# Kernel tuning notes

Hardware: AMD Instinct MI355X
Metric: run time of the kernel (lower is better)

Reference implementation:

```python
import jax, jax.numpy as jnp
import numpy as np

HEADS = 3
NEG_SLOPE = 0.2


def setup_inputs() -> dict:
    key = jax.random.key(0)
    ks = jax.random.split(key, 16)
    B, node_num, his, in_dim = 2, 5000, 12, 2
    N = B * node_num
    E = 160000
    hidden = 32
    C = hidden * his  # 384, per-head out channels of GATConv
    gat_in = in_dim * his  # 24
    s = 0.05
    return {
        "x": jax.random.normal(ks[0], (B, node_num, his, in_dim), jnp.float32),
        "edge_index": jax.random.randint(ks[1], (2, E), 0, N, jnp.int64),
        "lin_w": jax.random.normal(ks[2], (HEADS * C, gat_in), jnp.float32) * s,
        "att_src": jax.random.normal(ks[3], (HEADS, C), jnp.float32) * s,
        "att_dst": jax.random.normal(ks[4], (HEADS, C), jnp.float32) * s,
        "gat_bias": jax.random.normal(ks[5], (C,), jnp.float32) * s,
        "w_ih": jax.random.normal(ks[6], (3 * hidden, hidden), jnp.float32) * s,
        "w_hh": jax.random.normal(ks[7], (3 * hidden, hidden), jnp.float32) * s,
        "b_ih": jax.random.normal(ks[8], (3 * hidden,), jnp.float32) * s,
        "b_hh": jax.random.normal(ks[9], (3 * hidden,), jnp.float32) * s,
        "p1_w": jax.random.normal(ks[10], (1, hidden), jnp.float32) * s,
        "p1_b": jax.random.normal(ks[11], (1,), jnp.float32) * s,
        "p2_w": jax.random.normal(ks[12], (his, his), jnp.float32) * s,
        "p2_b": jax.random.normal(ks[13], (his,), jnp.float32) * s,
    }


def _gat_conv(xf, src, dst, N, lin_w, att_src, att_dst, gat_bias):
    # xf: [N, gat_in]; returns [N, C] (mean over heads, concat=False)
    heads, C = att_src.shape
    h = (xf @ lin_w.T).reshape(N, heads, C)           # [N,heads,C]
    a_src = jnp.einsum('nhc,hc->nh', h, att_src)      # [N,heads]
    a_dst = jnp.einsum('nhc,hc->nh', h, att_dst)
    alpha = jax.nn.leaky_relu(a_src[src] + a_dst[dst], NEG_SLOPE)  # [E,heads]
    # edge softmax over incoming edges of each dst node (stable)
    amax = jax.ops.segment_max(alpha, dst, num_segments=N)
    ea = jnp.exp(alpha - amax[dst])
    denom = jax.ops.segment_sum(ea, dst, num_segments=N)
    w = ea / denom[dst]                               # [E,heads]
    msg = h[src] * w[:, :, None]                      # [E,heads,C] -- dominant traffic
    out = jax.ops.segment_sum(msg, dst, num_segments=N)
    return out.mean(axis=1) + gat_bias                # [N,C]


def _gru(seq, w_ih, w_hh, b_ih, b_hh):
    # seq: [N, T, H] -> outputs [N, T, H], PyTorch GRU gate order (r,z,n)
    N, T, H = seq.shape
    def step(hprev, xt):
        gi = xt @ w_ih.T + b_ih
        gh = hprev @ w_hh.T + b_hh
        ir, iz, inn = jnp.split(gi, 3, axis=-1)
        hr, hz, hn = jnp.split(gh, 3, axis=-1)
        r = jax.nn.sigmoid(ir + hr)
        z = jax.nn.sigmoid(iz + hz)
        n = jnp.tanh(inn + r * hn)
        hnew = (1.0 - z) * n + z * hprev
        return hnew, hnew
    h0 = jnp.zeros((N, H), seq.dtype)
    _, hs = jax.lax.scan(step, h0, seq.transpose(1, 0, 2))
    return hs.transpose(1, 0, 2)


def reference(x, edge_index, lin_w, att_src, att_dst, gat_bias,
              w_ih, w_hh, b_ih, b_hh, p1_w, p1_b, p2_w, p2_b):
    B, node_num, his, in_dim = x.shape
    N = B * node_num
    xf = x.reshape(N, his * in_dim)
    # GATConv adds self-loops (add_self_loops=True default in PyG)
    loops = jnp.arange(N)
    src = jnp.concatenate([edge_index[0], loops])
    dst = jnp.concatenate([edge_index[1], loops])
    gat_out = _gat_conv(xf, src, dst, N, lin_w, att_src, att_dst, gat_bias)  # [N, hidden*his]
    hidden = w_hh.shape[1]
    gru_in = gat_out.reshape(N, his, hidden)
    gru_out = _gru(gru_in, w_ih, w_hh, b_ih, b_hh)    # [N, his, hidden]
    o = (gru_out @ p1_w.T + p1_b).squeeze(-1)         # [N, his]
    o = o @ p2_w.T + p2_b                              # [N, pred_num]
    return o.reshape(B, node_num, -1)
```

## Files before the change

### kernel.cpp

```cpp
#include <hip/hip_runtime.h>
#include <math.h>

#define HEADS 3
#define C_OUT 384
#define GAT_IN 24
#define HID 32
#define TSTEPS 12
#define NEG_SLOPE 0.2f
#define CAPW 64
#define SLOTS 96

typedef __attribute__((ext_vector_type(8))) short bf16x8;
typedef __attribute__((ext_vector_type(4))) float f32x4;

__device__ __forceinline__ float sigm(float x) {
  return 1.f / (1.f + __expf(-x));
}
__device__ __forceinline__ float tanh_fast(float x) {
  return 2.f / (1.f + __expf(-2.f * x)) - 1.f;
}
__device__ __forceinline__ unsigned short f2bf(float x) {
  unsigned int u = __float_as_uint(x);
  unsigned int r = u + 0x7fffu + ((u >> 16) & 1u);
  return (unsigned short)(r >> 16);
}
__device__ __forceinline__ unsigned int packbf(float lo, float hi) {
  return (unsigned int)f2bf(lo) | ((unsigned int)f2bf(hi) << 16);
}
__device__ __forceinline__ float bf_lo(unsigned int u) {
  return __uint_as_float(u << 16);
}
__device__ __forceinline__ float bf_hi(unsigned int u) {
  return __uint_as_float(u & 0xffff0000u);
}
__device__ __forceinline__ float bf2f(unsigned short u) {
  return __uint_as_float((unsigned int)u << 16);
}
__device__ __forceinline__ float lrelu(float x) {
  return x >= 0.f ? x : NEG_SLOPE * x;
}

__global__ __launch_bounds__(96) void k_const(const float* __restrict__ lin_w,
                                              const float* __restrict__ gat_bias,
                                              const float* __restrict__ wih,
                                              const float* __restrict__ bih,
                                              const float* __restrict__ att_src,
                                              const float* __restrict__ att_dst,
                                              unsigned short* __restrict__ WWf,
                                              float* __restrict__ biasb,
                                              float* __restrict__ vbuf,
                                              int* __restrict__ cnt, int N) {
  int b = blockIdx.x;
  if (b < 876) {
    int t = b / 73, kk = b % 73;
    int g = threadIdx.x;
    __shared__ float s_w[32];
    if (g < 32) {
      if (kk < 72) {
        int h = kk / 24, j = kk % 24;
        s_w[g] = lin_w[(size_t)(h * C_OUT + t * 32 + g) * GAT_IN + j] * (1.f / 3.f);
      } else {
        s_w[g] = gat_bias[t * 32 + g];
      }
    }
    __syncthreads();
    const float* wrow = wih + (size_t)g * 32;
    float acc = 0.f;
#pragma unroll
    for (int c = 0; c < 32; ++c) acc += s_w[c] * wrow[c];
    int nt = g >> 4, c2 = g & 15;
    if (kk < 72) {
      int q = kk >> 5, rem = kk & 31, hi2 = rem >> 3, j2 = rem & 7;
      WWf[((((size_t)t * 3 + q) * 6 + nt) * 64 + hi2 * 16 + c2) * 8 + j2] =
          f2bf(acc);
      if (kk < 24) {
        int remz = kk + 8, hiz = remz >> 3, jz = remz & 7;
        WWf[((((size_t)t * 3 + 2) * 6 + nt) * 64 + hiz * 16 + c2) * 8 + jz] = 0;
      }
    } else {
      biasb[t * 96 + g] = acc + bih[g];
    }
  } else if (b < 948) {
    int bb = b - 876;
    int h = bb / 24, j = bb % 24;
    int lane = threadIdx.x;
    if (lane >= 64) return;
    float as = 0.f, ad = 0.f;
    for (int c = lane; c < C_OUT; c += 64) {
      float wv = lin_w[(size_t)(h * C_OUT + c) * GAT_IN + j];
      as += att_src[h * C_OUT + c] * wv;
      ad += att_dst[h * C_OUT + c] * wv;
    }
#pragma unroll
    for (int off = 32; off >= 1; off >>= 1) {
      as += __shfl_xor(as, off, 64);
      ad += __shfl_xor(ad, off, 64);
    }
    if (lane == 0) {
      vbuf[h * 24 + j] = as;
      vbuf[72 + h * 24 + j] = ad;
    }
  } else {
    int i = (b - 948) * 96 + threadIdx.x;
    if (i < N) cnt[i] = 0;
  }
}

__global__ void k_place(const int* __restrict__ esrc,
                        const int* __restrict__ edst, int* __restrict__ cnt,
                        int* __restrict__ slist, int E, int ET) {
  int e = blockIdx.x * blockDim.x + threadIdx.x;
  if (e >= ET) return;
  int d, s;
  if (e < E) { d = edst[e]; s = esrc[e]; }
  else { d = e - E; s = e - E; }
  int pos = atomicAdd(&cnt[d], 1);
  if (pos < SLOTS) slist[(size_t)d * SLOTS + pos] = s;
}

__global__ __launch_bounds__(256) void k_aggx(
    const float* __restrict__ xf, const float* __restrict__ vbuf,
    const int* __restrict__ slist, const int* __restrict__ cnt,
    unsigned short* __restrict__ Yb, int N) {
  __shared__ float s_v[144];
  __shared__ float s_w[4][CAPW][3];
  __shared__ unsigned short s_xb[4][CAPW][26];
  int tid = threadIdx.x, lane = tid & 63, wv = tid >> 6;
  if (tid < 144) s_v[tid] = vbuf[tid];
  __syncthreads();
  int n = blockIdx.x * 4 + wv;
  if (n >= N) return;

  int deg = min(cnt[n], SLOTS);

  float xl = (lane < 24) ? xf[(size_t)n * 24 + lane] : 0.f;
  float ad0, ad1, ad2;
  {
    float p0 = (lane < 24) ? xl * s_v[72 + lane] : 0.f;
    float p1 = (lane < 24) ? xl * s_v[96 + lane] : 0.f;
    float p2 = (lane < 24) ? xl * s_v[120 + lane] : 0.f;
#pragma unroll
    for (int off = 32; off >= 1; off >>= 1) {
      p0 += __shfl_xor(p0, off, 64);
      p1 += __shfl_xor(p1, off, 64);
      p2 += __shfl_xor(p2, off, 64);
    }
    ad0 = p0; ad1 = p1; ad2 = p2;
  }

  float t0 = 0.f, t1 = 0.f, t2 = 0.f;
  for (int i = lane; i < deg; i += 64) {
    int s = slist[(size_t)n * SLOTS + i];
    const float4* xr = (const float4*)(xf + (size_t)s * 24);
    float xs[24];
#pragma unroll
    for (int q = 0; q < 6; ++q) {
      float4 v = xr[q];
      xs[4 * q] = v.x; xs[4 * q + 1] = v.y;
      xs[4 * q + 2] = v.z; xs[4 * q + 3] = v.w;
    }
    float as0 = 0.f, as1 = 0.f, as2 = 0.f;
#pragma unroll
    for (int j = 0; j < 24; ++j) {
      float v = xs[j];
      as0 += v * s_v[j];
      as1 += v * s_v[24 + j];
      as2 += v * s_v[48 + j];
    }
    float e0 = __expf(lrelu(as0 + ad0));
    float e1 = __expf(lrelu(as1 + ad1));
    float e2 = __expf(lrelu(as2 + ad2));
    if (i < CAPW) {
      s_w[wv][i][0] = e0; s_w[wv][i][1] = e1; s_w[wv][i][2] = e2;
#pragma unroll
      for (int j = 0; j < 24; ++j) s_xb[wv][i][j] = f2bf(xs[j]);
    }
    t0 += e0; t1 += e1; t2 += e2;
  }
#pragma unroll
  for (int off = 32; off >= 1; off >>= 1) {
    t0 += __shfl_xor(t0, off, 64);
    t1 += __shfl_xor(t1, off, 64);
    t2 += __shfl_xor(t2, off, 64);
  }
  float inv0 = 1.f / t0, inv1 = 1.f / t1, inv2 = 1.f / t2;

  int eg = lane >> 5;
  int c = lane & 31;
  float acc0 = 0.f, acc1 = 0.f, acc2 = 0.f;
  if (deg <= CAPW) {
    int cc = (c < 24) ? c : 0;
    float cmask = (c < 24) ? 1.f : 0.f;
#pragma unroll 2
    for (int i = eg; i < deg; i += 2) {
      float w0 = s_w[wv][i][0] * inv0;
      float w1 = s_w[wv][i][1] * inv1;
      float w2 = s_w[wv][i][2] * inv2;
      float xv = bf2f(s_xb[wv][i][cc]) * cmask;
      acc0 += w0 * xv; acc1 += w1 * xv; acc2 += w2 * xv;
    }
  } else {
    for (int i = eg; i < deg; i += 2) {
      int s = slist[(size_t)n * SLOTS + i];
      float as0 = 0.f, as1 = 0.f, as2 = 0.f;
      const float* xr = xf + (size_t)s * 24;
#pragma unroll
      for (int j = 0; j < 24; ++j) {
        float v = xr[j];
        as0 += v * s_v[j];
        as1 += v * s_v[24 + j];
        as2 += v * s_v[48 + j];
      }
      float w0 = __expf(lrelu(as0 + ad0)) * inv0;
      float w1 = __expf(lrelu(as1 + ad1)) * inv1;
      float w2 = __expf(lrelu(as2 + ad2)) * inv2;
      float xv = (c < 24) ? xf[(size_t)s * 24 + c] : 0.f;
      acc0 += w0 * xv; acc1 += w1 * xv; acc2 += w2 * xv;
    }
  }
  acc0 += __shfl_xor(acc0, 32, 64);
  acc1 += __shfl_xor(acc1, 32, 64);
  acc2 += __shfl_xor(acc2, 32, 64);
  if (lane < 24) {
    unsigned short* yr = Yb + (size_t)n * 72;
    yr[lane] = f2bf(acc0);
    yr[24 + lane] = f2bf(acc1);
    yr[48 + lane] = f2bf(acc2);
  }
}

__global__ __launch_bounds__(64) void k_rec2(
    const unsigned short* __restrict__ Yb,
    const unsigned short* __restrict__ WWf, const float* __restrict__ biasb,
    const float* __restrict__ whh, const float* __restrict__ bhh,
    const float* __restrict__ p1w, const float* __restrict__ p1b,
    const float* __restrict__ p2w, const float* __restrict__ p2b,
    float* __restrict__ out, int N) {
  __shared__ unsigned int gi_s[12][64][12];
  __shared__ float s_bias[12][96];
  __shared__ unsigned short h16[16][32];
  __shared__ float s_o[16][12];
  int l = threadIdx.x;
  int c = l & 15, hi = l >> 4;
  int m0 = blockIdx.x * 16;

  for (int u = l; u < 12 * 96; u += 64) s_bias[u / 96][u % 96] = biasb[u];

  int row = min(m0 + c, N - 1);
  const unsigned short* yr = Yb + (size_t)row * 72;
  bf16x8 ya0 = *(const bf16x8*)(yr + hi * 8);
  bf16x8 ya1 = *(const bf16x8*)(yr + 32 + hi * 8);
  bf16x8 ya2 = {0, 0, 0, 0, 0, 0, 0, 0};
  if (hi == 0) ya2 = *(const bf16x8*)(yr + 64);

  for (int t = 0; t < TSTEPS; ++t) {
    f32x4 g0 = {0,0,0,0}, g1 = {0,0,0,0}, g2 = {0,0,0,0};
    f32x4 g3 = {0,0,0,0}, g4 = {0,0,0,0}, g5 = {0,0,0,0};
#pragma unroll
    for (int q = 0; q < 3; ++q) {
      bf16x8 aq = (q == 0) ? ya0 : (q == 1) ? ya1 : ya2;
      const unsigned short* bp =
          WWf + ((((size_t)t * 3 + q) * 6) * 64 + l) * 8;
      bf16x8 b0 = *(const bf16x8*)(bp + 0 * 512);
      bf16x8 b1 = *(const bf16x8*)(bp + 1 * 512);
      bf16x8 b2 = *(const bf16x8*)(bp + 2 * 512);
      bf16x8 b3 = *(const bf16x8*)(bp + 3 * 512);
      bf16x8 b4 = *(const bf16x8*)(bp + 4 * 512);
      bf16x8 b5 = *(const bf16x8*)(bp + 5 * 512);
      g0 = __builtin_amdgcn_mfma_f32_16x16x32_bf16(aq, b0, g0, 0, 0, 0);
      g1 = __builtin_amdgcn_mfma_f32_16x16x32_bf16(aq, b1, g1, 0, 0, 0);
      g2 = __builtin_amdgcn_mfma_f32_16x16x32_bf16(aq, b2, g2, 0, 0, 0);
      g3 = __builtin_amdgcn_mfma_f32_16x16x32_bf16(aq, b3, g3, 0, 0, 0);
      g4 = __builtin_amdgcn_mfma_f32_16x16x32_bf16(aq, b4, g4, 0, 0, 0);
      g5 = __builtin_amdgcn_mfma_f32_16x16x32_bf16(aq, b5, g5, 0, 0, 0);
    }
    unsigned int* gp = &gi_s[t][l][0];
    gp[0] = packbf(g0[0], g0[1]);  gp[1] = packbf(g0[2], g0[3]);
    gp[2] = packbf(g1[0], g1[1]);  gp[3] = packbf(g1[2], g1[3]);
    gp[4] = packbf(g2[0], g2[1]);  gp[5] = packbf(g2[2], g2[3]);
    gp[6] = packbf(g3[0], g3[1]);  gp[7] = packbf(g3[2], g3[3]);
    gp[8] = packbf(g4[0], g4[1]);  gp[9] = packbf(g4[2], g4[3]);
    gp[10] = packbf(g5[0], g5[1]); gp[11] = packbf(g5[2], g5[3]);
  }

  bf16x8 wb[6];
#pragma unroll
  for (int nt = 0; nt < 6; ++nt) {
    const float* wp = whh + (size_t)(nt * 16 + c) * 32 + hi * 8;
#pragma unroll
    for (int j = 0; j < 8; ++j) wb[nt][j] = (short)f2bf(wp[j]);
  }

  float bhr0 = bhh[c], bhr1 = bhh[c + 16];
  float bhz0 = bhh[32 + c], bhz1 = bhh[48 + c];
  float bhn0 = bhh[64 + c], bhn1 = bhh[80 + c];
  float p1c0 = p1w[c], p1c1 = p1w[c + 16], p1b0 = p1b[0];

  float hA[4] = {0.f, 0.f, 0.f, 0.f}, hB[4] = {0.f, 0.f, 0.f, 0.f};
  bf16x8 ha = {0, 0, 0, 0, 0, 0, 0, 0};

  for (int t = 0; t < TSTEPS; ++t) {
    uint4 va = *(const uint4*)&gi_s[t][l][0];
    uint4 vb = *(const uint4*)&gi_s[t][l][4];
    uint4 vc = *(const uint4*)&gi_s[t][l][8];
    f32x4 zz = {0, 0, 0, 0};
    f32x4 h0 = __builtin_amdgcn_mfma_f32_16x16x32_bf16(ha, wb[0], zz, 0, 0, 0);
    f32x4 h1 = __builtin_amdgcn_mfma_f32_16x16x32_bf16(ha, wb[1], zz, 0, 0, 0);
    f32x4 h2 = __builtin_amdgcn_mfma_f32_16x16x32_bf16(ha, wb[2], zz, 0, 0, 0);
    f32x4 h3 = __builtin_amdgcn_mfma_f32_16x16x32_bf16(ha, wb[3], zz, 0, 0, 0);
    f32x4 h4 = __builtin_amdgcn_mfma_f32_16x16x32_bf16(ha, wb[4], zz, 0, 0, 0);
    f32x4 h5 = __builtin_amdgcn_mfma_f32_16x16x32_bf16(ha, wb[5], zz, 0, 0, 0);
    const float* bt = &s_bias[t][0];
    float br0 = bt[c], br1 = bt[16 + c];
    float bz0 = bt[32 + c], bz1 = bt[48 + c];
    float bn0 = bt[64 + c], bn1 = bt[80 + c];
    float g0v[4] = {bf_lo(va.x), bf_hi(va.x), bf_lo(va.y), bf_hi(va.y)};
    float g1v[4] = {bf_lo(va.z), bf_hi(va.z), bf_lo(va.w), bf_hi(va.w)};
    float g2v[4] = {bf_lo(vb.x), bf_hi(vb.x), bf_lo(vb.y), bf_hi(vb.y)};
    float g3v[4] = {bf_lo(vb.z), bf_hi(vb.z), bf_lo(vb.w), bf_hi(vb.w)};
    float g4v[4] = {bf_lo(vc.x), bf_hi(vc.x), bf_lo(vc.y), bf_hi(vc.y)};
    float g5v[4] = {bf_lo(vc.z), bf_hi(vc.z), bf_lo(vc.w), bf_hi(vc.w)};
    float po[4];
#pragma unroll
    for (int reg = 0; reg < 4; ++reg) {
      float r0 = sigm(g0v[reg] + br0 + h0[reg] + bhr0);
      float z0 = sigm(g2v[reg] + bz0 + h2[reg] + bhz0);
      float n0 = tanh_fast(g4v[reg] + bn0 + r0 * (h4[reg] + bhn0));
      hA[reg] = (1.f - z0) * n0 + z0 * hA[reg];
      float r1 = sigm(g1v[reg] + br1 + h1[reg] + bhr1);
      float z1 = sigm(g3v[reg] + bz1 + h3[reg] + bhz1);
      float n1 = tanh_fast(g5v[reg] + bn1 + r1 * (h5[reg] + bhn1));
      hB[reg] = (1.f - z1) * n1 + z1 * hB[reg];
      h16[hi * 4 + reg][c] = f2bf(hA[reg]);
      h16[hi * 4 + reg][c + 16] = f2bf(hB[reg]);
      po[reg] = p1c0 * hA[reg] + p1c1 * hB[reg];
    }
#pragma unroll
    for (int off = 1; off < 16; off <<= 1) {
#pragma unroll
      for (int reg = 0; reg < 4; ++reg) po[reg] += __shfl_xor(po[reg], off, 64);
    }
    if (c == 0) {
#pragma unroll
      for (int reg = 0; reg < 4; ++reg) s_o[hi * 4 + reg][t] = po[reg] + p1b0;
    }
    __syncthreads();
    ha = *(const bf16x8*)&h16[c][hi * 8];
  }
  __syncthreads();
  for (int idx = l; idx < 16 * TSTEPS; idx += 64) {
    int node = idx / TSTEPS, tt = idx % TSTEPS;
    int gn = m0 + node;
    if (gn < N) {
      float acc = p2b[tt];
#pragma unroll
      for (int s2 = 0; s2 < TSTEPS; ++s2)
        acc += p2w[tt * TSTEPS + s2] * s_o[node][s2];
      out[(size_t)gn * TSTEPS + tt] = acc;
    }
  }
}

extern "C" void kernel_launch(void* const* d_in, const int* in_sizes, int n_in,
                              void* d_out, int out_size, void* d_ws,
                              size_t ws_size, hipStream_t stream) {
  const float* x = (const float*)d_in[0];
  const int* ei = (const int*)d_in[1];
  const float* lin_w = (const float*)d_in[2];
  const float* att_src = (const float*)d_in[3];
  const float* att_dst = (const float*)d_in[4];
  const float* gat_bias = (const float*)d_in[5];
  const float* w_ih = (const float*)d_in[6];
  const float* w_hh = (const float*)d_in[7];
  const float* b_ih = (const float*)d_in[8];
  const float* b_hh = (const float*)d_in[9];
  const float* p1w = (const float*)d_in[10];
  const float* p1b = (const float*)d_in[11];
  const float* p2w = (const float*)d_in[12];
  const float* p2b = (const float*)d_in[13];

  int N = in_sizes[0] / GAT_IN;
  int E = in_sizes[1] / 2;
  int ET = E + N;

  size_t off = 0;
  char* base = (char*)d_ws;
  auto alloc = [&](size_t bytes) {
    void* p = base + off;
    off += (bytes + 255) & ~(size_t)255;
    return p;
  };
  unsigned short* Yb = (unsigned short*)alloc((size_t)N * 72 * 2);
  unsigned short* WWf = (unsigned short*)alloc((size_t)12 * 3 * 6 * 64 * 8 * 2);
  float* biasb = (float*)alloc((size_t)12 * 96 * 4);
  float* vbuf = (float*)alloc(144 * 4);
  int* cnt = (int*)alloc((size_t)N * 4);
  int* slist = (int*)alloc((size_t)N * SLOTS * 4);
  (void)ws_size; (void)n_in; (void)out_size;

  int zero_blocks = (N + 95) / 96;
  k_const<<<948 + zero_blocks, 96, 0, stream>>>(lin_w, gat_bias, w_ih, b_ih,
                                                att_src, att_dst, WWf, biasb,
                                                vbuf, cnt, N);
  k_place<<<(ET + 255) / 256, 256, 0, stream>>>(ei, ei + E, cnt, slist, E, ET);
  k_aggx<<<(N + 3) / 4, 256, 0, stream>>>(x, vbuf, slist, cnt, Yb, N);
  k_rec2<<<(N + 15) / 16, 64, 0, stream>>>(Yb, WWf, biasb, w_hh, b_hh, p1w,
                                           p1b, p2w, p2b, (float*)d_out, N);
}
```

Baseline: 79.25 us.

## Split GRU input projection into separate parallel kernel with prefetched recurrence

Moves the per-timestep input-gate projection out of the recurrent kernel into its own kernel launched over a (node-group, timestep) grid, writing bf16 gate pre-activations with the input bias folded in to a global buffer. The recurrent kernel then streams these from global memory, prefetching the next timestep's values while the current step computes. This exposes 12x more parallelism for the MFMA projection and shrinks the recurrent kernel's shared memory, which should raise occupancy. The cost is an extra launch and a global round-trip of roughly 7 MB of intermediate data.

```diff
diff --git a/kernel.cpp b/kernel.cpp
--- a/kernel.cpp
+++ b/kernel.cpp
@@ -229,23 +229,14 @@
   }
 }
 
-__global__ __launch_bounds__(64) void k_rec2(
+__global__ __launch_bounds__(64) void k_gi3(
     const unsigned short* __restrict__ Yb,
     const unsigned short* __restrict__ WWf, const float* __restrict__ biasb,
-    const float* __restrict__ whh, const float* __restrict__ bhh,
-    const float* __restrict__ p1w, const float* __restrict__ p1b,
-    const float* __restrict__ p2w, const float* __restrict__ p2b,
-    float* __restrict__ out, int N) {
-  __shared__ unsigned int gi_s[12][64][12];
-  __shared__ float s_bias[12][96];
-  __shared__ unsigned short h16[16][32];
-  __shared__ float s_o[16][12];
+    unsigned int* __restrict__ gig, int N) {
   int l = threadIdx.x;
   int c = l & 15, hi = l >> 4;
-  int m0 = blockIdx.x * 16;
-
-  for (int u = l; u < 12 * 96; u += 64) s_bias[u / 96][u % 96] = biasb[u];
-
+  int gblk = blockIdx.x, t = blockIdx.y;
+  int m0 = gblk * 16;
   int row = min(m0 + c, N - 1);
   const unsigned short* yr = Yb + (size_t)row * 72;
   bf16x8 ya0 = *(const bf16x8*)(yr + hi * 8);
@@ -253,35 +244,54 @@
   bf16x8 ya2 = {0, 0, 0, 0, 0, 0, 0, 0};
   if (hi == 0) ya2 = *(const bf16x8*)(yr + 64);
 
-  for (int t = 0; t < TSTEPS; ++t) {
-    f32x4 g0 = {0,0,0,0}, g1 = {0,0,0,0}, g2 = {0,0,0,0};
-    f32x4 g3 = {0,0,0,0}, g4 = {0,0,0,0}, g5 = {0,0,0,0};
-#pragma unroll
-    for (int q = 0; q < 3; ++q) {
-      bf16x8 aq = (q == 0) ? ya0 : (q == 1) ? ya1 : ya2;
-      const unsigned short* bp =
-          WWf + ((((size_t)t * 3 + q) * 6) * 64 + l) * 8;
-      bf16x8 b0 = *(const bf16x8*)(bp + 0 * 512);
-      bf16x8 b1 = *(const bf16x8*)(bp + 1 * 512);
-      bf16x8 b2 = *(const bf16x8*)(bp + 2 * 512);
-      bf16x8 b3 = *(const bf16x8*)(bp + 3 * 512);
-      bf16x8 b4 = *(const bf16x8*)(bp + 4 * 512);
-      bf16x8 b5 = *(const bf16x8*)(bp + 5 * 512);
-      g0 = __builtin_amdgcn_mfma_f32_16x16x32_bf16(aq, b0, g0, 0, 0, 0);
-      g1 = __builtin_amdgcn_mfma_f32_16x16x32_bf16(aq, b1, g1, 0, 0, 0);
-      g2 = __builtin_amdgcn_mfma_f32_16x16x32_bf16(aq, b2, g2, 0, 0, 0);
-      g3 = __builtin_amdgcn_mfma_f32_16x16x32_bf16(aq, b3, g3, 0, 0, 0);
-      g4 = __builtin_amdgcn_mfma_f32_16x16x32_bf16(aq, b4, g4, 0, 0, 0);
-      g5 = __builtin_amdgcn_mfma_f32_16x16x32_bf16(aq, b5, g5, 0, 0, 0);
-    }
-    unsigned int* gp = &gi_s[t][l][0];
-    gp[0] = packbf(g0[0], g0[1]);  gp[1] = packbf(g0[2], g0[3]);
-    gp[2] = packbf(g1[0], g1[1]);  gp[3] = packbf(g1[2], g1[3]);
-    gp[4] = packbf(g2[0], g2[1]);  gp[5] = packbf(g2[2], g2[3]);
-    gp[6] = packbf(g3[0], g3[1]);  gp[7] = packbf(g3[2], g3[3]);
-    gp[8] = packbf(g4[0], g4[1]);  gp[9] = packbf(g4[2], g4[3]);
-    gp[10] = packbf(g5[0], g5[1]); gp[11] = packbf(g5[2], g5[3]);
-  }
+  f32x4 g0 = {0,0,0,0}, g1 = {0,0,0,0}, g2 = {0,0,0,0};
+  f32x4 g3 = {0,0,0,0}, g4 = {0,0,0,0}, g5 = {0,0,0,0};
+#pragma unroll
+  for (int q = 0; q < 3; ++q) {
+    bf16x8 aq = (q == 0) ? ya0 : (q == 1) ? ya1 : ya2;
+    const unsigned short* bp = WWf + ((((size_t)t * 3 + q) * 6) * 64 + l) * 8;
+    bf16x8 b0 = *(const bf16x8*)(bp + 0 * 512);
+    bf16x8 b1 = *(const bf16x8*)(bp + 1 * 512);
+    bf16x8 b2 = *(const bf16x8*)(bp + 2 * 512);
+    bf16x8 b3 = *(const bf16x8*)(bp + 3 * 512);
+    bf16x8 b4 = *(const bf16x8*)(bp + 4 * 512);
+    bf16x8 b5 = *(const bf16x8*)(bp + 5 * 512);
+    g0 = __builtin_amdgcn_mfma_f32_16x16x32_bf16(aq, b0, g0, 0, 0, 0);
+    g1 = __builtin_amdgcn_mfma_f32_16x16x32_bf16(aq, b1, g1, 0, 0, 0);
+    g2 = __builtin_amdgcn_mfma_f32_16x16x32_bf16(aq, b2, g2, 0, 0, 0);
+    g3 = __builtin_amdgcn_mfma_f32_16x16x32_bf16(aq, b3, g3, 0, 0, 0);
+    g4 = __builtin_amdgcn_mfma_f32_16x16x32_bf16(aq, b4, g4, 0, 0, 0);
+    g5 = __builtin_amdgcn_mfma_f32_16x16x32_bf16(aq, b5, g5, 0, 0, 0);
+  }
+  const float* bt = biasb + t * 96;
+  float b0s = bt[0 * 16 + c], b1s = bt[1 * 16 + c], b2s = bt[2 * 16 + c];
+  float b3s = bt[3 * 16 + c], b4s = bt[4 * 16 + c], b5s = bt[5 * 16 + c];
+  unsigned int* gp = gig + (size_t)(gblk * 12 + t) * 768;
+  gp[0 * 64 + l] = packbf(g0[0] + b0s, g0[1] + b0s);
+  gp[1 * 64 + l] = packbf(g0[2] + b0s, g0[3] + b0s);
+  gp[2 * 64 + l] = packbf(g1[0] + b1s, g1[1] + b1s);
+  gp[3 * 64 + l] = packbf(g1[2] + b1s, g1[3] + b1s);
+  gp[4 * 64 + l] = packbf(g2[0] + b2s, g2[1] + b2s);
+  gp[5 * 64 + l] = packbf(g2[2] + b2s, g2[3] + b2s);
+  gp[6 * 64 + l] = packbf(g3[0] + b3s, g3[1] + b3s);
+  gp[7 * 64 + l] = packbf(g3[2] + b3s, g3[3] + b3s);
+  gp[8 * 64 + l] = packbf(g4[0] + b4s, g4[1] + b4s);
+  gp[9 * 64 + l] = packbf(g4[2] + b4s, g4[3] + b4s);
+  gp[10 * 64 + l] = packbf(g5[0] + b5s, g5[1] + b5s);
+  gp[11 * 64 + l] = packbf(g5[2] + b5s, g5[3] + b5s);
+}
+
+__global__ __launch_bounds__(64) void k_rec3(
+    const unsigned int* __restrict__ gig, const float* __restrict__ whh,
+    const float* __restrict__ bhh, const float* __restrict__ p1w,
+    const float* __restrict__ p1b, const float* __restrict__ p2w,
+    const float* __restrict__ p2b, float* __restrict__ out, int N) {
+  __shared__ unsigned short h16[16][32];
+  __shared__ float s_o[16][12];
+  int l = threadIdx.x;
+  int c = l & 15, hi = l >> 4;
+  int gblk = blockIdx.x;
+  int m0 = gblk * 16;
 
   bf16x8 wb[6];
 #pragma unroll
@@ -299,10 +309,21 @@
   float hA[4] = {0.f, 0.f, 0.f, 0.f}, hB[4] = {0.f, 0.f, 0.f, 0.f};
   bf16x8 ha = {0, 0, 0, 0, 0, 0, 0, 0};
 
+  const unsigned int* gp = gig + (size_t)gblk * 12 * 768;
+  unsigned int cur[12];
+#pragma unroll
+  for (int i = 0; i < 12; ++i) cur[i] = gp[i * 64 + l];
+
   for (int t = 0; t < TSTEPS; ++t) {
-    uint4 va = *(const uint4*)&gi_s[t][l][0];
-    uint4 vb = *(const uint4*)&gi_s[t][l][4];
-    uint4 vc = *(const uint4*)&gi_s[t][l][8];
+    unsigned int nxt[12];
+    if (t + 1 < TSTEPS) {
+      const unsigned int* gpn = gp + (t + 1) * 768;
+#pragma unroll
+      for (int i = 0; i < 12; ++i) nxt[i] = gpn[i * 64 + l];
+    } else {
+#pragma unroll
+      for (int i = 0; i < 12; ++i) nxt[i] = 0;
+    }
     f32x4 zz = {0, 0, 0, 0};
     f32x4 h0 = __builtin_amdgcn_mfma_f32_16x16x32_bf16(ha, wb[0], zz, 0, 0, 0);
     f32x4 h1 = __builtin_amdgcn_mfma_f32_16x16x32_bf16(ha, wb[1], zz, 0, 0, 0);
@@ -310,26 +331,23 @@
     f32x4 h3 = __builtin_amdgcn_mfma_f32_16x16x32_bf16(ha, wb[3], zz, 0, 0, 0);
     f32x4 h4 = __builtin_amdgcn_mfma_f32_16x16x32_bf16(ha, wb[4], zz, 0, 0, 0);
     f32x4 h5 = __builtin_amdgcn_mfma_f32_16x16x32_bf16(ha, wb[5], zz, 0, 0, 0);
-    const float* bt = &s_bias[t][0];
-    float br0 = bt[c], br1 = bt[16 + c];
-    float bz0 = bt[32 + c], bz1 = bt[48 + c];
-    float bn0 = bt[64 + c], bn1 = bt[80 + c];
-    float g0v[4] = {bf_lo(va.x), bf_hi(va.x), bf_lo(va.y), bf_hi(va.y)};
-    float g1v[4] = {bf_lo(va.z), bf_hi(va.z), bf_lo(va.w), bf_hi(va.w)};
-    float g2v[4] = {bf_lo(vb.x), bf_hi(vb.x), bf_lo(vb.y), bf_hi(vb.y)};
-    float g3v[4] = {bf_lo(vb.z), bf_hi(vb.z), bf_lo(vb.w), bf_hi(vb.w)};
-    float g4v[4] = {bf_lo(vc.x), bf_hi(vc.x), bf_lo(vc.y), bf_hi(vc.y)};
-    float g5v[4] = {bf_lo(vc.z), bf_hi(vc.z), bf_lo(vc.w), bf_hi(vc.w)};
+    float g0v[4] = {bf_lo(cur[0]), bf_hi(cur[0]), bf_lo(cur[1]), bf_hi(cur[1])};
+    float g1v[4] = {bf_lo(cur[2]), bf_hi(cur[2]), bf_lo(cur[3]), bf_hi(cur[3])};
+    float g2v[4] = {bf_lo(cur[4]), bf_hi(cur[4]), bf_lo(cur[5]), bf_hi(cur[5])};
+    float g3v[4] = {bf_lo(cur[6]), bf_hi(cur[6]), bf_lo(cur[7]), bf_hi(cur[7])};
+    float g4v[4] = {bf_lo(cur[8]), bf_hi(cur[8]), bf_lo(cur[9]), bf_hi(cur[9])};
+    float g5v[4] = {bf_lo(cur[10]), bf_hi(cur[10]), bf_lo(cur[11]),
+                    bf_hi(cur[11])};
     float po[4];
 #pragma unroll
     for (int reg = 0; reg < 4; ++reg) {
-      float r0 = sigm(g0v[reg] + br0 + h0[reg] + bhr0);
-      float z0 = sigm(g2v[reg] + bz0 + h2[reg] + bhz0);
-      float n0 = tanh_fast(g4v[reg] + bn0 + r0 * (h4[reg] + bhn0));
+      float r0 = sigm(g0v[reg] + h0[reg] + bhr0);
+      float z0 = sigm(g2v[reg] + h2[reg] + bhz0);
+      float n0 = tanh_fast(g4v[reg] + r0 * (h4[reg] + bhn0));
       hA[reg] = (1.f - z0) * n0 + z0 * hA[reg];
-      float r1 = sigm(g1v[reg] + br1 + h1[reg] + bhr1);
-      float z1 = sigm(g3v[reg] + bz1 + h3[reg] + bhz1);
-      float n1 = tanh_fast(g5v[reg] + bn1 + r1 * (h5[reg] + bhn1));
+      float r1 = sigm(g1v[reg] + h1[reg] + bhr1);
+      float z1 = sigm(g3v[reg] + h3[reg] + bhz1);
+      float n1 = tanh_fast(g5v[reg] + r1 * (h5[reg] + bhn1));
       hB[reg] = (1.f - z1) * n1 + z1 * hB[reg];
       h16[hi * 4 + reg][c] = f2bf(hA[reg]);
       h16[hi * 4 + reg][c + 16] = f2bf(hB[reg]);
@@ -346,6 +364,8 @@
     }
     __syncthreads();
     ha = *(const bf16x8*)&h16[c][hi * 8];
+#pragma unroll
+    for (int i = 0; i < 12; ++i) cur[i] = nxt[i];
   }
   __syncthreads();
   for (int idx = l; idx < 16 * TSTEPS; idx += 64) {
@@ -382,6 +402,7 @@
   int N = in_sizes[0] / GAT_IN;
   int E = in_sizes[1] / 2;
   int ET = E + N;
+  int NG = (N + 15) / 16;
 
   size_t off = 0;
   char* base = (char*)d_ws;
@@ -392,6 +413,7 @@
   };
   unsigned short* Yb = (unsigned short*)alloc((size_t)N * 72 * 2);
   unsigned short* WWf = (unsigned short*)alloc((size_t)12 * 3 * 6 * 64 * 8 * 2);
+  unsigned int* gig = (unsigned int*)alloc((size_t)NG * 12 * 768 * 4);
   float* biasb = (float*)alloc((size_t)12 * 96 * 4);
   float* vbuf = (float*)alloc(144 * 4);
   int* cnt = (int*)alloc((size_t)N * 4);
@@ -404,6 +426,7 @@
                                                 vbuf, cnt, N);
   k_place<<<(ET + 255) / 256, 256, 0, stream>>>(ei, ei + E, cnt, slist, E, ET);
   k_aggx<<<(N + 3) / 4, 256, 0, stream>>>(x, vbuf, slist, cnt, Yb, N);
-  k_rec2<<<(N + 15) / 16, 64, 0, stream>>>(Yb, WWf, biasb, w_hh, b_hh, p1w,
-                                           p1b, p2w, p2b, (float*)d_out, N);
-}
+  k_gi3<<<dim3(NG, 12), 64, 0, stream>>>(Yb, WWf, biasb, gig, N);
+  k_rec3<<<NG, 64, 0, stream>>>(gig, w_hh, b_hh, p1w, p1b, p2w, p2b,
+                                (float*)d_out, N);
+}
```

Result: no change. 80.31 us (+1.3%).

## Fuse GAT aggregation and GRU recurrence into one 512-thread kernel

Applied to the files above, without the earlier changes.

Merges the attention-aggregation kernel and the GRU kernel into a single kernel with 16 nodes per 512-thread block. The aggregated features stay in LDS instead of making a global round trip, and the input-gate MFMAs are split across 8 waves. Neighbour features are now re-gathered from global memory by source index instead of being cached as bf16 in LDS. The sequential recurrence runs on wave 0 only while the other seven waves sit idle at barriers, which risks low utilisation during that phase.

```diff
diff --git a/kernel.cpp b/kernel.cpp
--- a/kernel.cpp
+++ b/kernel.cpp
@@ -1,7 +1,6 @@
 #include <hip/hip_runtime.h>
 #include <math.h>
 
-#define HEADS 3
 #define C_OUT 384
 #define GAT_IN 24
 #define HID 32
@@ -32,9 +31,6 @@
 }
 __device__ __forceinline__ float bf_hi(unsigned int u) {
   return __uint_as_float(u & 0xffff0000u);
-}
-__device__ __forceinline__ float bf2f(unsigned short u) {
-  return __uint_as_float((unsigned int)u << 16);
 }
 __device__ __forceinline__ float lrelu(float x) {
   return x >= 0.f ? x : NEG_SLOPE * x;
@@ -118,237 +114,238 @@
   if (pos < SLOTS) slist[(size_t)d * SLOTS + pos] = s;
 }
 
-__global__ __launch_bounds__(256) void k_aggx(
+__global__ __launch_bounds__(512, 2) void k_fused(
     const float* __restrict__ xf, const float* __restrict__ vbuf,
     const int* __restrict__ slist, const int* __restrict__ cnt,
-    unsigned short* __restrict__ Yb, int N) {
-  __shared__ float s_v[144];
-  __shared__ float s_w[4][CAPW][3];
-  __shared__ unsigned short s_xb[4][CAPW][26];
-  int tid = threadIdx.x, lane = tid & 63, wv = tid >> 6;
-  if (tid < 144) s_v[tid] = vbuf[tid];
-  __syncthreads();
-  int n = blockIdx.x * 4 + wv;
-  if (n >= N) return;
-
-  int deg = min(cnt[n], SLOTS);
-
-  float xl = (lane < 24) ? xf[(size_t)n * 24 + lane] : 0.f;
-  float ad0, ad1, ad2;
-  {
-    float p0 = (lane < 24) ? xl * s_v[72 + lane] : 0.f;
-    float p1 = (lane < 24) ? xl * s_v[96 + lane] : 0.f;
-    float p2 = (lane < 24) ? xl * s_v[120 + lane] : 0.f;
-#pragma unroll
-    for (int off = 32; off >= 1; off >>= 1) {
-      p0 += __shfl_xor(p0, off, 64);
-      p1 += __shfl_xor(p1, off, 64);
-      p2 += __shfl_xor(p2, off, 64);
-    }
-    ad0 = p0; ad1 = p1; ad2 = p2;
-  }
-
-  float t0 = 0.f, t1 = 0.f, t2 = 0.f;
-  for (int i = lane; i < deg; i += 64) {
-    int s = slist[(size_t)n * SLOTS + i];
-    const float4* xr = (const float4*)(xf + (size_t)s * 24);
-    float xs[24];
-#pragma unroll
-    for (int q = 0; q < 6; ++q) {
-      float4 v = xr[q];
-      xs[4 * q] = v.x; xs[4 * q + 1] = v.y;
-      xs[4 * q + 2] = v.z; xs[4 * q + 3] = v.w;
-    }
-    float as0 = 0.f, as1 = 0.f, as2 = 0.f;
-#pragma unroll
-    for (int j = 0; j < 24; ++j) {
-      float v = xs[j];
-      as0 += v * s_v[j];
-      as1 += v * s_v[24 + j];
-      as2 += v * s_v[48 + j];
-    }
-    float e0 = __expf(lrelu(as0 + ad0));
-    float e1 = __expf(lrelu(as1 + ad1));
-    float e2 = __expf(lrelu(as2 + ad2));
-    if (i < CAPW) {
-      s_w[wv][i][0] = e0; s_w[wv][i][1] = e1; s_w[wv][i][2] = e2;
-#pragma unroll
-      for (int j = 0; j < 24; ++j) s_xb[wv][i][j] = f2bf(xs[j]);
-    }
-    t0 += e0; t1 += e1; t2 += e2;
-  }
-#pragma unroll
-  for (int off = 32; off >= 1; off >>= 1) {
-    t0 += __shfl_xor(t0, off, 64);
-    t1 += __shfl_xor(t1, off, 64);
-    t2 += __shfl_xor(t2, off, 64);
-  }
-  float inv0 = 1.f / t0, inv1 = 1.f / t1, inv2 = 1.f / t2;
-
-  int eg = lane >> 5;
-  int c = lane & 31;
-  float acc0 = 0.f, acc1 = 0.f, acc2 = 0.f;
-  if (deg <= CAPW) {
-    int cc = (c < 24) ? c : 0;
-    float cmask = (c < 24) ? 1.f : 0.f;
-#pragma unroll 2
-    for (int i = eg; i < deg; i += 2) {
-      float w0 = s_w[wv][i][0] * inv0;
-      float w1 = s_w[wv][i][1] * inv1;
-      float w2 = s_w[wv][i][2] * inv2;
-      float xv = bf2f(s_xb[wv][i][cc]) * cmask;
-      acc0 += w0 * xv; acc1 += w1 * xv; acc2 += w2 * xv;
-    }
-  } else {
-    for (int i = eg; i < deg; i += 2) {
-      int s = slist[(size_t)n * SLOTS + i];
-      float as0 = 0.f, as1 = 0.f, as2 = 0.f;
-      const float* xr = xf + (size_t)s * 24;
-#pragma unroll
-      for (int j = 0; j < 24; ++j) {
-        float v = xr[j];
-        as0 += v * s_v[j];
-        as1 += v * s_v[24 + j];
-        as2 += v * s_v[48 + j];
-      }
-      float w0 = __expf(lrelu(as0 + ad0)) * inv0;
-      float w1 = __expf(lrelu(as1 + ad1)) * inv1;
-      float w2 = __expf(lrelu(as2 + ad2)) * inv2;
-      float xv = (c < 24) ? xf[(size_t)s * 24 + c] : 0.f;
-      acc0 += w0 * xv; acc1 += w1 * xv; acc2 += w2 * xv;
-    }
-  }
-  acc0 += __shfl_xor(acc0, 32, 64);
-  acc1 += __shfl_xor(acc1, 32, 64);
-  acc2 += __shfl_xor(acc2, 32, 64);
-  if (lane < 24) {
-    unsigned short* yr = Yb + (size_t)n * 72;
-    yr[lane] = f2bf(acc0);
-    yr[24 + lane] = f2bf(acc1);
-    yr[48 + lane] = f2bf(acc2);
-  }
-}
-
-__global__ __launch_bounds__(64) void k_rec2(
-    const unsigned short* __restrict__ Yb,
     const unsigned short* __restrict__ WWf, const float* __restrict__ biasb,
     const float* __restrict__ whh, const float* __restrict__ bhh,
     const float* __restrict__ p1w, const float* __restrict__ p1b,
     const float* __restrict__ p2w, const float* __restrict__ p2b,
     float* __restrict__ out, int N) {
-  __shared__ unsigned int gi_s[12][64][12];
-  __shared__ float s_bias[12][96];
+  __shared__ float s_v[144];
+  __shared__ int s_src[16][CAPW];
+  __shared__ float s_w[16][CAPW][3];
+  __shared__ unsigned short Ybf[16][72];
+  __shared__ unsigned int gi_lds[TSTEPS][12][64];
   __shared__ unsigned short h16[16][32];
   __shared__ float s_o[16][12];
-  int l = threadIdx.x;
-  int c = l & 15, hi = l >> 4;
+  int tid = threadIdx.x, l = tid & 63, wv = tid >> 6;
   int m0 = blockIdx.x * 16;
 
-  for (int u = l; u < 12 * 96; u += 64) s_bias[u / 96][u % 96] = biasb[u];
-
-  int row = min(m0 + c, N - 1);
-  const unsigned short* yr = Yb + (size_t)row * 72;
-  bf16x8 ya0 = *(const bf16x8*)(yr + hi * 8);
-  bf16x8 ya1 = *(const bf16x8*)(yr + 32 + hi * 8);
-  bf16x8 ya2 = {0, 0, 0, 0, 0, 0, 0, 0};
-  if (hi == 0) ya2 = *(const bf16x8*)(yr + 64);
-
-  for (int t = 0; t < TSTEPS; ++t) {
-    f32x4 g0 = {0,0,0,0}, g1 = {0,0,0,0}, g2 = {0,0,0,0};
-    f32x4 g3 = {0,0,0,0}, g4 = {0,0,0,0}, g5 = {0,0,0,0};
-#pragma unroll
-    for (int q = 0; q < 3; ++q) {
-      bf16x8 aq = (q == 0) ? ya0 : (q == 1) ? ya1 : ya2;
-      const unsigned short* bp =
-          WWf + ((((size_t)t * 3 + q) * 6) * 64 + l) * 8;
-      bf16x8 b0 = *(const bf16x8*)(bp + 0 * 512);
-      bf16x8 b1 = *(const bf16x8*)(bp + 1 * 512);
-      bf16x8 b2 = *(const bf16x8*)(bp + 2 * 512);
-      bf16x8 b3 = *(const bf16x8*)(bp + 3 * 512);
-      bf16x8 b4 = *(const bf16x8*)(bp + 4 * 512);
-      bf16x8 b5 = *(const bf16x8*)(bp + 5 * 512);
-      g0 = __builtin_amdgcn_mfma_f32_16x16x32_bf16(aq, b0, g0, 0, 0, 0);
-      g1 = __builtin_amdgcn_mfma_f32_16x16x32_bf16(aq, b1, g1, 0, 0, 0);
-      g2 = __builtin_amdgcn_mfma_f32_16x16x32_bf16(aq, b2, g2, 0, 0, 0);
-      g3 = __builtin_amdgcn_mfma_f32_16x16x32_bf16(aq, b3, g3, 0, 0, 0);
-      g4 = __builtin_amdgcn_mfma_f32_16x16x32_bf16(aq, b4, g4, 0, 0, 0);
-      g5 = __builtin_amdgcn_mfma_f32_16x16x32_bf16(aq, b5, g5, 0, 0, 0);
-    }
-    unsigned int* gp = &gi_s[t][l][0];
-    gp[0] = packbf(g0[0], g0[1]);  gp[1] = packbf(g0[2], g0[3]);
-    gp[2] = packbf(g1[0], g1[1]);  gp[3] = packbf(g1[2], g1[3]);
-    gp[4] = packbf(g2[0], g2[1]);  gp[5] = packbf(g2[2], g2[3]);
-    gp[6] = packbf(g3[0], g3[1]);  gp[7] = packbf(g3[2], g3[3]);
-    gp[8] = packbf(g4[0], g4[1]);  gp[9] = packbf(g4[2], g4[3]);
-    gp[10] = packbf(g5[0], g5[1]); gp[11] = packbf(g5[2], g5[3]);
-  }
-
-  bf16x8 wb[6];
-#pragma unroll
-  for (int nt = 0; nt < 6; ++nt) {
-    const float* wp = whh + (size_t)(nt * 16 + c) * 32 + hi * 8;
-#pragma unroll
-    for (int j = 0; j < 8; ++j) wb[nt][j] = (short)f2bf(wp[j]);
-  }
-
-  float bhr0 = bhh[c], bhr1 = bhh[c + 16];
-  float bhz0 = bhh[32 + c], bhz1 = bhh[48 + c];
-  float bhn0 = bhh[64 + c], bhn1 = bhh[80 + c];
-  float p1c0 = p1w[c], p1c1 = p1w[c + 16], p1b0 = p1b[0];
-
-  float hA[4] = {0.f, 0.f, 0.f, 0.f}, hB[4] = {0.f, 0.f, 0.f, 0.f};
-  bf16x8 ha = {0, 0, 0, 0, 0, 0, 0, 0};
-
-  for (int t = 0; t < TSTEPS; ++t) {
-    uint4 va = *(const uint4*)&gi_s[t][l][0];
-    uint4 vb = *(const uint4*)&gi_s[t][l][4];
-    uint4 vc = *(const uint4*)&gi_s[t][l][8];
-    f32x4 zz = {0, 0, 0, 0};
-    f32x4 h0 = __builtin_amdgcn_mfma_f32_16x16x32_bf16(ha, wb[0], zz, 0, 0, 0);
-    f32x4 h1 = __builtin_amdgcn_mfma_f32_16x16x32_bf16(ha, wb[1], zz, 0, 0, 0);
-    f32x4 h2 = __builtin_amdgcn_mfma_f32_16x16x32_bf16(ha, wb[2], zz, 0, 0, 0);
-    f32x4 h3 = __builtin_amdgcn_mfma_f32_16x16x32_bf16(ha, wb[3], zz, 0, 0, 0);
-    f32x4 h4 = __builtin_amdgcn_mfma_f32_16x16x32_bf16(ha, wb[4], zz, 0, 0, 0);
-    f32x4 h5 = __builtin_amdgcn_mfma_f32_16x16x32_bf16(ha, wb[5], zz, 0, 0, 0);
-    const float* bt = &s_bias[t][0];
-    float br0 = bt[c], br1 = bt[16 + c];
-    float bz0 = bt[32 + c], bz1 = bt[48 + c];
-    float bn0 = bt[64 + c], bn1 = bt[80 + c];
-    float g0v[4] = {bf_lo(va.x), bf_hi(va.x), bf_lo(va.y), bf_hi(va.y)};
-    float g1v[4] = {bf_lo(va.z), bf_hi(va.z), bf_lo(va.w), bf_hi(va.w)};
-    float g2v[4] = {bf_lo(vb.x), bf_hi(vb.x), bf_lo(vb.y), bf_hi(vb.y)};
-    float g3v[4] = {bf_lo(vb.z), bf_hi(vb.z), bf_lo(vb.w), bf_hi(vb.w)};
-    float g4v[4] = {bf_lo(vc.x), bf_hi(vc.x), bf_lo(vc.y), bf_hi(vc.y)};
-    float g5v[4] = {bf_lo(vc.z), bf_hi(vc.z), bf_lo(vc.w), bf_hi(vc.w)};
-    float po[4];
-#pragma unroll
-    for (int reg = 0; reg < 4; ++reg) {
-      float r0 = sigm(g0v[reg] + br0 + h0[reg] + bhr0);
-      float z0 = sigm(g2v[reg] + bz0 + h2[reg] + bhz0);
-      float n0 = tanh_fast(g4v[reg] + bn0 + r0 * (h4[reg] + bhn0));
-      hA[reg] = (1.f - z0) * n0 + z0 * hA[reg];
-      float r1 = sigm(g1v[reg] + br1 + h1[reg] + bhr1);
-      float z1 = sigm(g3v[reg] + bz1 + h3[reg] + bhz1);
-      float n1 = tanh_fast(g5v[reg] + bn1 + r1 * (h5[reg] + bhn1));
-      hB[reg] = (1.f - z1) * n1 + z1 * hB[reg];
-      h16[hi * 4 + reg][c] = f2bf(hA[reg]);
-      h16[hi * 4 + reg][c + 16] = f2bf(hB[reg]);
-      po[reg] = p1c0 * hA[reg] + p1c1 * hB[reg];
-    }
-#pragma unroll
-    for (int off = 1; off < 16; off <<= 1) {
-#pragma unroll
-      for (int reg = 0; reg < 4; ++reg) po[reg] += __shfl_xor(po[reg], off, 64);
-    }
-    if (c == 0) {
-#pragma unroll
-      for (int reg = 0; reg < 4; ++reg) s_o[hi * 4 + reg][t] = po[reg] + p1b0;
-    }
-    __syncthreads();
-    ha = *(const bf16x8*)&h16[c][hi * 8];
+  if (tid < 144) s_v[tid] = vbuf[tid];
+  __syncthreads();
+
+  for (int ii = 0; ii < 2; ++ii) {
+    int slot = (wv << 1) | ii;
+    int n = m0 + slot;
+    bool act = n < N;
+    int nc = act ? n : 0;
+    int deg = act ? min(cnt[nc], SLOTS) : 0;
+
+    float xl = (l < 24) ? xf[(size_t)nc * 24 + l] : 0.f;
+    float q0 = (l < 24) ? xl * s_v[72 + l] : 0.f;
+    float q1 = (l < 24) ? xl * s_v[96 + l] : 0.f;
+    float q2 = (l < 24) ? xl * s_v[120 + l] : 0.f;
+#pragma unroll
+    for (int off = 32; off >= 1; off >>= 1) {
+      q0 += __shfl_xor(q0, off, 64);
+      q1 += __shfl_xor(q1, off, 64);
+      q2 += __shfl_xor(q2, off, 64);
+    }
+    float ad0 = q0, ad1 = q1, ad2 = q2;
+
+    float t0 = 0.f, t1 = 0.f, t2 = 0.f;
+    for (int i = l; i < deg; i += 64) {
+      int s = slist[(size_t)nc * SLOTS + i];
+      const float4* xr = (const float4*)(xf + (size_t)s * 24);
+      float xs[24];
+#pragma unroll
+      for (int q = 0; q < 6; ++q) {
+        float4 v = xr[q];
+        xs[4 * q] = v.x; xs[4 * q + 1] = v.y;
+        xs[4 * q + 2] = v.z; xs[4 * q + 3] = v.w;
+      }
+      float as0 = 0.f, as1 = 0.f, as2 = 0.f;
+#pragma unroll
+      for (int j = 0; j < 24; ++j) {
+        float v = xs[j];
+        as0 += v * s_v[j];
+        as1 += v * s_v[24 + j];
+        as2 += v * s_v[48 + j];
+      }
+      float e0 = __expf(lrelu(as0 + ad0));
+      float e1 = __expf(lrelu(as1 + ad1));
+      float e2 = __expf(lrelu(as2 + ad2));
+      if (i < CAPW) {
+        s_src[slot][i] = s;
+        s_w[slot][i][0] = e0; s_w[slot][i][1] = e1; s_w[slot][i][2] = e2;
+      }
+      t0 += e0; t1 += e1; t2 += e2;
+    }
+#pragma unroll
+    for (int off = 32; off >= 1; off >>= 1) {
+      t0 += __shfl_xor(t0, off, 64);
+      t1 += __shfl_xor(t1, off, 64);
+      t2 += __shfl_xor(t2, off, 64);
+    }
+    float inv0 = 1.f / t0, inv1 = 1.f / t1, inv2 = 1.f / t2;
+
+    int eg = l >> 5, c = l & 31;
+    float a0 = 0.f, a1 = 0.f, a2 = 0.f;
+    if (deg <= CAPW) {
+      for (int i = eg; i < deg; i += 2) {
+        int s = s_src[slot][i];
+        float w0 = s_w[slot][i][0] * inv0;
+        float w1 = s_w[slot][i][1] * inv1;
+        float w2 = s_w[slot][i][2] * inv2;
+        float xv = (c < 24) ? xf[(size_t)s * 24 + c] : 0.f;
+        a0 += w0 * xv; a1 += w1 * xv; a2 += w2 * xv;
+      }
+    } else {
+      for (int i = eg; i < deg; i += 2) {
+        int s = slist[(size_t)nc * SLOTS + i];
+        float as0 = 0.f, as1 = 0.f, as2 = 0.f;
+        const float* xr = xf + (size_t)s * 24;
+#pragma unroll
+        for (int j = 0; j < 24; ++j) {
+          float v = xr[j];
+          as0 += v * s_v[j];
+          as1 += v * s_v[24 + j];
+          as2 += v * s_v[48 + j];
+        }
+        float w0 = __expf(lrelu(as0 + ad0)) * inv0;
+        float w1 = __expf(lrelu(as1 + ad1)) * inv1;
+        float w2 = __expf(lrelu(as2 + ad2)) * inv2;
+        float xv = (c < 24) ? xf[(size_t)s * 24 + c] : 0.f;
+        a0 += w0 * xv; a1 += w1 * xv; a2 += w2 * xv;
+      }
+    }
+    a0 += __shfl_xor(a0, 32, 64);
+    a1 += __shfl_xor(a1, 32, 64);
+    a2 += __shfl_xor(a2, 32, 64);
+    if (act && l < 24) {
+      Ybf[slot][l] = f2bf(a0);
+      Ybf[slot][24 + l] = f2bf(a1);
+      Ybf[slot][48 + l] = f2bf(a2);
+    }
   }
   __syncthreads();
-  for (int idx = l; idx < 16 * TSTEPS; idx += 64) {
+
+  {
+    int c = l & 15, hi = l >> 4;
+    bf16x8 ya0 = *(const bf16x8*)&Ybf[c][hi * 8];
+    bf16x8 ya1 = *(const bf16x8*)&Ybf[c][32 + hi * 8];
+    bf16x8 ya2 = {0, 0, 0, 0, 0, 0, 0, 0};
+    if (hi == 0) ya2 = *(const bf16x8*)&Ybf[c][64];
+    for (int t = wv; t < TSTEPS; t += 8) {
+      f32x4 g0 = {0,0,0,0}, g1 = {0,0,0,0}, g2 = {0,0,0,0};
+      f32x4 g3 = {0,0,0,0}, g4 = {0,0,0,0}, g5 = {0,0,0,0};
+#pragma unroll
+      for (int q = 0; q < 3; ++q) {
+        bf16x8 aq = (q == 0) ? ya0 : (q == 1) ? ya1 : ya2;
+        const unsigned short* bp =
+            WWf + ((((size_t)t * 3 + q) * 6) * 64 + l) * 8;
+        bf16x8 b0 = *(const bf16x8*)(bp + 0 * 512);
+        bf16x8 b1 = *(const bf16x8*)(bp + 1 * 512);
+        bf16x8 b2 = *(const bf16x8*)(bp + 2 * 512);
+        bf16x8 b3 = *(const bf16x8*)(bp + 3 * 512);
+        bf16x8 b4 = *(const bf16x8*)(bp + 4 * 512);
+        bf16x8 b5 = *(const bf16x8*)(bp + 5 * 512);
+        g0 = __builtin_amdgcn_mfma_f32_16x16x32_bf16(aq, b0, g0, 0, 0, 0);
+        g1 = __builtin_amdgcn_mfma_f32_16x16x32_bf16(aq, b1, g1, 0, 0, 0);
+        g2 = __builtin_amdgcn_mfma_f32_16x16x32_bf16(aq, b2, g2, 0, 0, 0);
+        g3 = __builtin_amdgcn_mfma_f32_16x16x32_bf16(aq, b3, g3, 0, 0, 0);
+        g4 = __builtin_amdgcn_mfma_f32_16x16x32_bf16(aq, b4, g4, 0, 0, 0);
+        g5 = __builtin_amdgcn_mfma_f32_16x16x32_bf16(aq, b5, g5, 0, 0, 0);
+      }
+      const float* bt = biasb + t * 96;
+      float b0s = bt[c], b1s = bt[16 + c], b2s = bt[32 + c];
+      float b3s = bt[48 + c], b4s = bt[64 + c], b5s = bt[80 + c];
+      gi_lds[t][0][l] = packbf(g0[0] + b0s, g0[1] + b0s);
+      gi_lds[t][1][l] = packbf(g0[2] + b0s, g0[3] + b0s);
+      gi_lds[t][2][l] = packbf(g1[0] + b1s, g1[1] + b1s);
+      gi_lds[t][3][l] = packbf(g1[2] + b1s, g1[3] + b1s);
+      gi_lds[t][4][l] = packbf(g2[0] + b2s, g2[1] + b2s);
+      gi_lds[t][5][l] = packbf(g2[2] + b2s, g2[3] + b2s);
+      gi_lds[t][6][l] = packbf(g3[0] + b3s, g3[1] + b3s);
+      gi_lds[t][7][l] = packbf(g3[2] + b3s, g3[3] + b3s);
+      gi_lds[t][8][l] = packbf(g4[0] + b4s, g4[1] + b4s);
+      gi_lds[t][9][l] = packbf(g4[2] + b4s, g4[3] + b4s);
+      gi_lds[t][10][l] = packbf(g5[0] + b5s, g5[1] + b5s);
+      gi_lds[t][11][l] = packbf(g5[2] + b5s, g5[3] + b5s);
+    }
+  }
+  __syncthreads();
+
+  {
+    int c = l & 15, hi = l >> 4;
+    bf16x8 wb[6];
+#pragma unroll
+    for (int nt = 0; nt < 6; ++nt) {
+      const float* wp = whh + (size_t)(nt * 16 + c) * 32 + hi * 8;
+#pragma unroll
+      for (int j = 0; j < 8; ++j) wb[nt][j] = (short)f2bf(wp[j]);
+    }
+    float bhr0 = bhh[c], bhr1 = bhh[c + 16];
+    float bhz0 = bhh[32 + c], bhz1 = bhh[48 + c];
+    float bhn0 = bhh[64 + c], bhn1 = bhh[80 + c];
+    float p1c0 = p1w[c], p1c1 = p1w[c + 16], p1b0 = p1b[0];
+    float hA[4] = {0.f, 0.f, 0.f, 0.f}, hB[4] = {0.f, 0.f, 0.f, 0.f};
+    bf16x8 ha = {0, 0, 0, 0, 0, 0, 0, 0};
+
+    for (int t = 0; t < TSTEPS; ++t) {
+      if (wv == 0) {
+        unsigned int cu[12];
+#pragma unroll
+        for (int i = 0; i < 12; ++i) cu[i] = gi_lds[t][i][l];
+        f32x4 zz = {0, 0, 0, 0};
+        f32x4 h0 = __builtin_amdgcn_mfma_f32_16x16x32_bf16(ha, wb[0], zz, 0, 0, 0);
+        f32x4 h1 = __builtin_amdgcn_mfma_f32_16x16x32_bf16(ha, wb[1], zz, 0, 0, 0);
+        f32x4 h2 = __builtin_amdgcn_mfma_f32_16x16x32_bf16(ha, wb[2], zz, 0, 0, 0);
+        f32x4 h3 = __builtin_amdgcn_mfma_f32_16x16x32_bf16(ha, wb[3], zz, 0, 0, 0);
+        f32x4 h4 = __builtin_amdgcn_mfma_f32_16x16x32_bf16(ha, wb[4], zz, 0, 0, 0);
+        f32x4 h5 = __builtin_amdgcn_mfma_f32_16x16x32_bf16(ha, wb[5], zz, 0, 0, 0);
+        float g0v[4] = {bf_lo(cu[0]), bf_hi(cu[0]), bf_lo(cu[1]), bf_hi(cu[1])};
+        float g1v[4] = {bf_lo(cu[2]), bf_hi(cu[2]), bf_lo(cu[3]), bf_hi(cu[3])};
+        float g2v[4] = {bf_lo(cu[4]), bf_hi(cu[4]), bf_lo(cu[5]), bf_hi(cu[5])};
+        float g3v[4] = {bf_lo(cu[6]), bf_hi(cu[6]), bf_lo(cu[7]), bf_hi(cu[7])};
+        float g4v[4] = {bf_lo(cu[8]), bf_hi(cu[8]), bf_lo(cu[9]), bf_hi(cu[9])};
+        float g5v[4] = {bf_lo(cu[10]), bf_hi(cu[10]), bf_lo(cu[11]),
+                        bf_hi(cu[11])};
+        float po[4];
+#pragma unroll
+        for (int reg = 0; reg < 4; ++reg) {
+          float r0 = sigm(g0v[reg] + h0[reg] + bhr0);
+          float z0 = sigm(g2v[reg] + h2[reg] + bhz0);
+          float n0 = tanh_fast(g4v[reg] + r0 * (h4[reg] + bhn0));
+          hA[reg] = (1.f - z0) * n0 + z0 * hA[reg];
+          float r1 = sigm(g1v[reg] + h1[reg] + bhr1);
+          float z1 = sigm(g3v[reg] + h3[reg] + bhz1);
+          float n1 = tanh_fast(g5v[reg] + r1 * (h5[reg] + bhn1));
+          hB[reg] = (1.f - z1) * n1 + z1 * hB[reg];
+          h16[hi * 4 + reg][c] = f2bf(hA[reg]);
+          h16[hi * 4 + reg][c + 16] = f2bf(hB[reg]);
+          po[reg] = p1c0 * hA[reg] + p1c1 * hB[reg];
+        }
+#pragma unroll
+        for (int off = 1; off < 16; off <<= 1) {
+#pragma unroll
+          for (int reg = 0; reg < 4; ++reg)
+            po[reg] += __shfl_xor(po[reg], off, 64);
+        }
+        if (c == 0) {
+#pragma unroll
+          for (int reg = 0; reg < 4; ++reg)
+            s_o[hi * 4 + reg][t] = po[reg] + p1b0;
+        }
+      }
+      __syncthreads();
+      if (wv == 0) ha = *(const bf16x8*)&h16[c][hi * 8];
+    }
+  }
+  __syncthreads();
+
+  for (int idx = tid; idx < 16 * TSTEPS; idx += 512) {
     int node = idx / TSTEPS, tt = idx % TSTEPS;
     int gn = m0 + node;
     if (gn < N) {
@@ -382,6 +379,7 @@
   int N = in_sizes[0] / GAT_IN;
   int E = in_sizes[1] / 2;
   int ET = E + N;
+  int NG = (N + 15) / 16;
 
   size_t off = 0;
   char* base = (char*)d_ws;
@@ -390,7 +388,6 @@
     off += (bytes + 255) & ~(size_t)255;
     return p;
   };
-  unsigned short* Yb = (unsigned short*)alloc((size_t)N * 72 * 2);
   unsigned short* WWf = (unsigned short*)alloc((size_t)12 * 3 * 6 * 64 * 8 * 2);
   float* biasb = (float*)alloc((size_t)12 * 96 * 4);
   float* vbuf = (float*)alloc(144 * 4);
@@ -403,7 +400,6 @@
                                                 att_src, att_dst, WWf, biasb,
                                                 vbuf, cnt, N);
   k_place<<<(ET + 255) / 256, 256, 0, stream>>>(ei, ei + E, cnt, slist, E, ET);
-  k_aggx<<<(N + 3) / 4, 256, 0, stream>>>(x, vbuf, slist, cnt, Yb, N);
-  k_rec2<<<(N + 15) / 16, 64, 0, stream>>>(Yb, WWf, biasb, w_hh, b_hh, p1w,
-                                           p1b, p2w, p2b, (float*)d_out, N);
-}
+  k_fused<<<NG, 512, 0, stream>>>(x, vbuf, slist, cnt, WWf, biasb, w_hh, b_hh,
+                                  p1w, p1b, p2w, p2b, (float*)d_out, N);
+}
```

New measurement: 101.6 us. 1.28x slower.
